# Kernel tuning notes

Hardware: AMD Instinct MI355X
Metric: run time of the kernel (lower is better)

Reference implementation:

```python
import jax, jax.numpy as jnp
import numpy as np

BN_EPS = 1e-5


def sparsemax(z):
    # z: [B, D]; sparse projection onto the simplex along last axis.
    D = z.shape[-1]
    z_sorted = jnp.flip(jnp.sort(z, axis=-1), axis=-1)          # descending
    cs = jnp.cumsum(z_sorted, axis=-1)                           # cumulative sums
    k = jnp.arange(1, D + 1, dtype=z.dtype)                      # 1..D
    support = (1.0 + k * z_sorted) > cs                          # support condition
    k_star = jnp.sum(support, axis=-1, keepdims=True)            # support size, int
    cs_k = jnp.take_along_axis(cs, k_star - 1, axis=-1)
    tau = (cs_k - 1.0) / k_star.astype(z.dtype)                  # threshold
    return jnp.maximum(z - tau, 0.0)


def setup_inputs() -> dict:
    key = jax.random.key(0)
    k1, k2, k3 = jax.random.split(key, 3)
    B, D = 32768, 1024
    a = jax.random.normal(k1, (B, D), dtype=jnp.float32)
    p = jax.random.uniform(k2, (B, D), dtype=jnp.float32)        # prior scales in (0,1)
    W = jax.random.normal(k3, (D, D), dtype=jnp.float32) * (1.0 / np.sqrt(D))
    b = jnp.zeros((D,), dtype=jnp.float32)
    gamma = jnp.ones((D,), dtype=jnp.float32)
    beta = jnp.zeros((D,), dtype=jnp.float32)
    return {"a": a, "p": p, "W": W, "b": b, "gamma": gamma, "beta": beta}


def reference(a, p, W, b, gamma, beta):
    # Linear: a @ W^T + b  (torch nn.Linear convention)
    h = jnp.einsum("bd,ed->be", a, W) + b
    # BatchNorm1d (training mode: batch stats, biased variance)
    mean = jnp.mean(h, axis=0)
    var = jnp.mean(jnp.square(h - mean), axis=0)
    h = (h - mean) * jax.lax.rsqrt(var + BN_EPS) * gamma + beta
    # Prior scaling, then sparsemax -> attention mask
    mask = sparsemax(p * h)
    return mask
```

## Files before the change

kernel.cpp:

```cpp
#include <hip/hip_runtime.h>
#include <hip/hip_fp16.h>
#include <stdint.h>

typedef _Float16 f16x8 __attribute__((ext_vector_type(8)));
typedef _Float16 f16x2 __attribute__((ext_vector_type(2)));
typedef float f32x4 __attribute__((ext_vector_type(4)));

#define BM 128
#define BN 128
#define BK 64

#define GBM 256
#define GBN 256
#define GBK 32

__device__ __forceinline__ void async_copy16(const void* g, void* l) {
  __builtin_amdgcn_global_load_lds(
      (__attribute__((address_space(1))) void*)(g),
      (__attribute__((address_space(3))) void*)(l),
      16, 0, 0);
}

__global__ __launch_bounds__(256) void cvt_f32_f16(const float* __restrict__ in,
                                                   _Float16* __restrict__ out,
                                                   size_t n8) {
  const size_t stride = (size_t)gridDim.x * 256;
  for (size_t i = (size_t)blockIdx.x * 256 + threadIdx.x; i < n8; i += stride) {
    const float4* s = (const float4*)in + i * 2;
    float4 u = s[0];
    float4 v = s[1];
    f16x8 h;
    h[0] = (_Float16)u.x; h[1] = (_Float16)u.y; h[2] = (_Float16)u.z; h[3] = (_Float16)u.w;
    h[4] = (_Float16)v.x; h[5] = (_Float16)v.y; h[6] = (_Float16)v.z; h[7] = (_Float16)v.w;
    ((f16x8*)out)[i] = h;
  }
}

__device__ __forceinline__ void stage32(const _Float16* __restrict__ src,
                                        _Float16* __restrict__ dst,
                                        int K, int wave, int lane) {
#pragma unroll
  for (int i = 0; i < 2; ++i) {
    const int basechunk = i * 512 + wave * 64;
    const int g   = basechunk + lane;
    const int row = g >> 2;
    const int sc  = (g & 3) ^ ((row >> 1) & 3);
    async_copy16(src + (size_t)row * K + sc * 8, dst + basechunk * 8);
  }
}

__global__ __launch_bounds__(512, 2) void gemm16(const _Float16* __restrict__ Ah,
                                                 const _Float16* __restrict__ Wh,
                                                 const float* __restrict__ bias,
                                                 _Float16* __restrict__ Hout,
                                                 float* __restrict__ psum,
                                                 float* __restrict__ psumsq,
                                                 int M, int N, int K) {
  __shared__ __attribute__((aligned(16))) _Float16 lsA[4][GBM * GBK];
  __shared__ __attribute__((aligned(16))) _Float16 lsB[4][GBN * GBK];

  const int tid  = threadIdx.x;
  const int wave = tid >> 6;
  const int lane = tid & 63;
  const int l16  = lane & 15;
  const int quad = lane >> 4;
  const int wr   = wave >> 2;
  const int wc   = wave & 3;

  const int li  = blockIdx.x;
  const int xcd = li & 7;
  const int jj  = li >> 3;
  const int bnT = jj & 3;
  const int bmT = xcd + (jj >> 2) * 8;
  const int bm  = bmT * GBM;
  const int bn  = bnT * GBN;

  const _Float16* Ag = Ah + (size_t)bm * K;
  const _Float16* Bg = Wh + (size_t)bn * K;

  f32x4 acc[8][4];
#pragma unroll
  for (int i = 0; i < 8; ++i)
#pragma unroll
    for (int j = 0; j < 4; ++j) acc[i][j] = (f32x4){0.f, 0.f, 0.f, 0.f};

  const int NT = K >> 5;

#pragma unroll
  for (int t = 0; t < 3; ++t) {
    stage32(Ag + t * GBK, lsA[t], K, wave, lane);
    stage32(Bg + t * GBK, lsB[t], K, wave, lane);
  }
  asm volatile("s_waitcnt vmcnt(8)" ::: "memory");
  __builtin_amdgcn_s_barrier();
  __builtin_amdgcn_sched_barrier(0);

  const int pos   = quad ^ ((l16 >> 1) & 3);
  const int abase = ((wr * 128 + l16) * 4 + pos) * 8;
  const int bbase = ((wc * 64 + l16) * 4 + pos) * 8;

#pragma unroll 1
  for (int t = 0; t < NT; ++t) {
    const _Float16* bufA = lsA[t & 3];
    const _Float16* bufB = lsB[t & 3];
    const int tp = t + 3;
    const bool st = tp < NT;

    if (st) stage32(Ag + (size_t)tp * GBK, lsA[tp & 3], K, wave, lane);
    f16x8 bf[4], af[4];
#pragma unroll
    for (int j = 0; j < 4; ++j) bf[j] = *(const f16x8*)&bufB[bbase + j * 512];
#pragma unroll
    for (int i = 0; i < 4; ++i) af[i] = *(const f16x8*)&bufA[abase + i * 512];
    __builtin_amdgcn_s_barrier();
    asm volatile("s_waitcnt lgkmcnt(0)" ::: "memory");
    __builtin_amdgcn_sched_barrier(0);
    __builtin_amdgcn_s_setprio(1);
#pragma unroll
    for (int i = 0; i < 4; ++i)
#pragma unroll
      for (int j = 0; j < 4; ++j)
        acc[i][j] = __builtin_amdgcn_mfma_f32_16x16x32_f16(af[i], bf[j], acc[i][j], 0, 0, 0);
    __builtin_amdgcn_s_setprio(0);
    __builtin_amdgcn_s_barrier();
    __builtin_amdgcn_sched_barrier(0);

    if (st) stage32(Bg + (size_t)tp * GBK, lsB[tp & 3], K, wave, lane);
    f16x8 af2[4];
#pragma unroll
    for (int i = 0; i < 4; ++i) af2[i] = *(const f16x8*)&bufA[abase + (i + 4) * 512];
    __builtin_amdgcn_s_barrier();
    asm volatile("s_waitcnt lgkmcnt(0)" ::: "memory");
    __builtin_amdgcn_sched_barrier(0);
    __builtin_amdgcn_s_setprio(1);
#pragma unroll
    for (int i = 0; i < 4; ++i)
#pragma unroll
      for (int j = 0; j < 4; ++j)
        acc[i + 4][j] = __builtin_amdgcn_mfma_f32_16x16x32_f16(af2[i], bf[j], acc[i + 4][j], 0, 0, 0);
    __builtin_amdgcn_s_setprio(0);

    if (t < NT - 3)       asm volatile("s_waitcnt vmcnt(8)" ::: "memory");
    else if (t == NT - 3) asm volatile("s_waitcnt vmcnt(4)" ::: "memory");
    else if (t == NT - 2) asm volatile("s_waitcnt vmcnt(0)" ::: "memory");
    __builtin_amdgcn_s_barrier();
    __builtin_amdgcn_sched_barrier(0);
  }

  f16x2* H2 = (f16x2*)Hout;
#pragma unroll
  for (int j = 0; j < 4; ++j) {
    const int c = bn + wc * 64 + j * 16 + l16;
    const float bv = bias[c];
    float s = 0.f, s2 = 0.f;
#pragma unroll
    for (int i = 0; i < 8; ++i) {
      const int r = bm + wr * 128 + i * 16 + quad * 4;
      f32x4 v = acc[i][j];
      const float v0 = v[0] + bv, v1 = v[1] + bv, v2 = v[2] + bv, v3 = v[3] + bv;
      s  += v0 + v1 + v2 + v3;
      s2 += v0 * v0 + v1 * v1 + v2 * v2 + v3 * v3;
      const size_t d0 = (size_t)(r >> 1) * N + c;
      H2[d0]     = (f16x2){(_Float16)v0, (_Float16)v1};
      H2[d0 + N] = (f16x2){(_Float16)v2, (_Float16)v3};
    }
    s  += __shfl_xor(s, 16, 64);  s  += __shfl_xor(s, 32, 64);
    s2 += __shfl_xor(s2, 16, 64); s2 += __shfl_xor(s2, 32, 64);
    if (quad == 0) {
      const size_t slot = (size_t)(bmT * 2 + wr) * N + c;
      psum[slot]   = s;
      psumsq[slot] = s2;
    }
  }
}

__global__ __launch_bounds__(256) void gemm_fallback(const float* __restrict__ Af,
                                                     const float* __restrict__ Wf,
                                                     const float* __restrict__ bias,
                                                     float* __restrict__ C,
                                                     float* __restrict__ sum,
                                                     float* __restrict__ sumsq,
                                                     int M, int N, int K) {
  __shared__ __attribute__((aligned(16))) _Float16 lsA[BM * BK];
  __shared__ __attribute__((aligned(16))) _Float16 lsB[BN * BK];
  const int tid  = threadIdx.x;
  const int wave = tid >> 6;
  const int lane = tid & 63;
  const int wrow = (wave >> 1) * 64;
  const int wcol = (wave & 1) * 64;
  const int l16  = lane & 15;
  const int quad = lane >> 4;
  const int bm = blockIdx.y * BM;
  const int bn = blockIdx.x * BN;

  f32x4 acc[4][4];
#pragma unroll
  for (int i = 0; i < 4; ++i)
#pragma unroll
    for (int j = 0; j < 4; ++j) acc[i][j] = (f32x4){0.f, 0.f, 0.f, 0.f};

  for (int k0 = 0; k0 < K; k0 += BK) {
#pragma unroll
    for (int i = 0; i < 4; ++i) {
      const int g   = i * 256 + tid;
      const int row = g >> 3;
      const int kc8 = g & 7;
      const int slot = row * 8 + (kc8 ^ (row & 7));
      {
        const float* src = Af + (size_t)(bm + row) * K + k0 + kc8 * 8;
        float4 u = *(const float4*)src;
        float4 v = *(const float4*)(src + 4);
        f16x8 h;
        h[0] = (_Float16)u.x; h[1] = (_Float16)u.y; h[2] = (_Float16)u.z; h[3] = (_Float16)u.w;
        h[4] = (_Float16)v.x; h[5] = (_Float16)v.y; h[6] = (_Float16)v.z; h[7] = (_Float16)v.w;
        *(f16x8*)&lsA[slot * 8] = h;
      }
      {
        const float* src = Wf + (size_t)(bn + row) * K + k0 + kc8 * 8;
        float4 u = *(const float4*)src;
        float4 v = *(const float4*)(src + 4);
        f16x8 h;
        h[0] = (_Float16)u.x; h[1] = (_Float16)u.y; h[2] = (_Float16)u.z; h[3] = (_Float16)u.w;
        h[4] = (_Float16)v.x; h[5] = (_Float16)v.y; h[6] = (_Float16)v.z; h[7] = (_Float16)v.w;
        *(f16x8*)&lsB[slot * 8] = h;
      }
    }
    __syncthreads();
#pragma unroll
    for (int kk = 0; kk < BK; kk += 32) {
      f16x8 af[4], bf[4];
#pragma unroll
      for (int i = 0; i < 4; ++i) {
        const int r = wrow + i * 16 + l16;
        const int col = ((kk >> 3) + quad) ^ (l16 & 7);
        af[i] = *(const f16x8*)&lsA[r * 64 + col * 8];
      }
#pragma unroll
      for (int j = 0; j < 4; ++j) {
        const int r = wcol + j * 16 + l16;
        const int col = ((kk >> 3) + quad) ^ (l16 & 7);
        bf[j] = *(const f16x8*)&lsB[r * 64 + col * 8];
      }
#pragma unroll
      for (int i = 0; i < 4; ++i)
#pragma unroll
        for (int j = 0; j < 4; ++j)
          acc[i][j] = __builtin_amdgcn_mfma_f32_16x16x32_f16(af[i], bf[j], acc[i][j], 0, 0, 0);
    }
    __syncthreads();
  }

#pragma unroll
  for (int j = 0; j < 4; ++j) {
    const int c = bn + wcol + j * 16 + l16;
    const float bv = bias[c];
    float s = 0.f, s2 = 0.f;
#pragma unroll
    for (int i = 0; i < 4; ++i) {
      const int r = bm + wrow + i * 16 + quad * 4;
      float* Cp = C + (size_t)r * N + c;
      f32x4 v = acc[i][j];
#pragma unroll
      for (int rr = 0; rr < 4; ++rr) {
        float val = v[rr] + bv;
        Cp[(size_t)rr * N] = val;
        s += val;
        s2 += val * val;
      }
    }
    s  += __shfl_xor(s, 16, 64);  s  += __shfl_xor(s, 32, 64);
    s2 += __shfl_xor(s2, 16, 64); s2 += __shfl_xor(s2, 32, 64);
    if (quad == 0) {
      atomicAdd(&sum[c], s);
      atomicAdd(&sumsq[c], s2);
    }
  }
}

__global__ __launch_bounds__(256) void bn_finalize_wave(const float* __restrict__ psum,
                                                        const float* __restrict__ psumsq,
                                                        const float* __restrict__ gamma,
                                                        const float* __restrict__ beta,
                                                        float* __restrict__ scale,
                                                        float* __restrict__ shift,
                                                        float invB, int S, int D) {
  const int wave = threadIdx.x >> 6;
  const int lane = threadIdx.x & 63;
  const int c = blockIdx.x * 4 + wave;
  float s = 0.f, q = 0.f;
  for (int u = lane; u < S; u += 64) {
    s += psum[(size_t)u * D + c];
    q += psumsq[(size_t)u * D + c];
  }
#pragma unroll
  for (int o = 32; o > 0; o >>= 1) {
    s += __shfl_xor(s, o, 64);
    q += __shfl_xor(q, o, 64);
  }
  if (lane == 0) {
    float mean = s * invB;
    float var  = q * invB - mean * mean;
    float rstd = rsqrtf(var + 1e-5f);
    float sc = rstd * gamma[c];
    scale[c] = sc;
    shift[c] = beta[c] - mean * sc;
  }
}

__global__ __launch_bounds__(256) void bn_finalize(const float* __restrict__ sum,
                                                   const float* __restrict__ sumsq,
                                                   const float* __restrict__ gamma,
                                                   const float* __restrict__ beta,
                                                   float* __restrict__ scale,
                                                   float* __restrict__ shift,
                                                   float invB) {
  const int c = blockIdx.x * 256 + threadIdx.x;
  float mean = sum[c] * invB;
  float var  = sumsq[c] * invB - mean * mean;
  float rstd = rsqrtf(var + 1e-5f);
  float sc = rstd * gamma[c];
  scale[c] = sc;
  shift[c] = beta[c] - mean * sc;
}

__global__ __launch_bounds__(256) void bn_sparsemax_h2(const _Float16* __restrict__ H2,
                                                       const float* __restrict__ P,
                                                       const float* __restrict__ scale,
                                                       const float* __restrict__ shift,
                                                       float* __restrict__ out, int D) {
  const int wave = threadIdx.x >> 6;
  const int lane = threadIdx.x & 63;
  const int row = blockIdx.x * 4 + wave;
  const int rp  = row >> 1;
  const int par = row & 1;

  const f16x8* Hc = (const f16x8*)(H2 + (size_t)rp * 2 * D);
  const f32x4* P4 = (const f32x4*)(P + (size_t)row * D);
  const f32x4* SC = (const f32x4*)scale;
  const f32x4* SH = (const f32x4*)shift;

  f32x4 z[4];
  float tot = 0.f;
#pragma unroll
  for (int j = 0; j < 4; ++j) {
    const int idx = j * 64 + lane;
    f16x8 h = Hc[idx];
    f32x4 hv = {(float)h[par], (float)h[2 + par], (float)h[4 + par], (float)h[6 + par]};
    f32x4 zz = P4[idx] * (hv * SC[idx] + SH[idx]);
    z[j] = zz;
    tot += zz[0] + zz[1] + zz[2] + zz[3];
  }
#pragma unroll
  for (int o = 32; o > 0; o >>= 1) tot += __shfl_xor(tot, o, 64);

  float tau = (tot - 1.0f) / (float)D;
  float kprev = -1.0f;
  for (int it = 0; it < 64; ++it) {
    float s = 0.f, kf = 0.f;
#pragma unroll
    for (int j = 0; j < 4; ++j)
#pragma unroll
      for (int c = 0; c < 4; ++c) {
        float zz = z[j][c];
        if (zz > tau) { s += zz; kf += 1.0f; }
      }
#pragma unroll
    for (int o = 32; o > 0; o >>= 1) {
      s  += __shfl_xor(s, o, 64);
      kf += __shfl_xor(kf, o, 64);
    }
    tau = (s - 1.0f) / kf;
    if (kf == kprev) break;
    kprev = kf;
  }

  f32x4* O4 = (f32x4*)(out + (size_t)row * D);
#pragma unroll
  for (int j = 0; j < 4; ++j) {
    const int idx = j * 64 + lane;
    f32x4 o;
#pragma unroll
    for (int c = 0; c < 4; ++c) o[c] = fmaxf(z[j][c] - tau, 0.f);
    O4[idx] = o;
  }
}

__global__ __launch_bounds__(256) void bn_sparsemax_f32(const float* __restrict__ H,
                                                        const float* __restrict__ P,
                                                        const float* __restrict__ scale,
                                                        const float* __restrict__ shift,
                                                        float* __restrict__ out, int D) {
  const int wave = threadIdx.x >> 6;
  const int lane = threadIdx.x & 63;
  const int row = blockIdx.x * 4 + wave;
  const size_t rowoff = (size_t)row * D;
  const f32x4* H4 = (const f32x4*)(H + rowoff);
  const f32x4* P4 = (const f32x4*)(P + rowoff);
  const f32x4* SC = (const f32x4*)scale;
  const f32x4* SH = (const f32x4*)shift;

  f32x4 z[4];
  float tot = 0.f;
#pragma unroll
  for (int j = 0; j < 4; ++j) {
    const int idx = j * 64 + lane;
    f32x4 zz = P4[idx] * (H4[idx] * SC[idx] + SH[idx]);
    z[j] = zz;
    tot += zz[0] + zz[1] + zz[2] + zz[3];
  }
#pragma unroll
  for (int o = 32; o > 0; o >>= 1) tot += __shfl_xor(tot, o, 64);

  float tau = (tot - 1.0f) / (float)D;
  float kprev = -1.0f;
  for (int it = 0; it < 64; ++it) {
    float s = 0.f, kf = 0.f;
#pragma unroll
    for (int j = 0; j < 4; ++j)
#pragma unroll
      for (int c = 0; c < 4; ++c) {
        float zz = z[j][c];
        if (zz > tau) { s += zz; kf += 1.0f; }
      }
#pragma unroll
    for (int o = 32; o > 0; o >>= 1) {
      s  += __shfl_xor(s, o, 64);
      kf += __shfl_xor(kf, o, 64);
    }
    tau = (s - 1.0f) / kf;
    if (kf == kprev) break;
    kprev = kf;
  }

  f32x4* O4 = (f32x4*)(out + rowoff);
#pragma unroll
  for (int j = 0; j < 4; ++j) {
    const int idx = j * 64 + lane;
    f32x4 o;
#pragma unroll
    for (int c = 0; c < 4; ++c) o[c] = fmaxf(z[j][c] - tau, 0.f);
    O4[idx] = o;
  }
}

extern "C" void kernel_launch(void* const* d_in, const int* in_sizes, int n_in,
                              void* d_out, int out_size, void* d_ws, size_t ws_size,
                              hipStream_t stream) {
  const float* a     = (const float*)d_in[0];
  const float* p     = (const float*)d_in[1];
  const float* W     = (const float*)d_in[2];
  const float* b     = (const float*)d_in[3];
  const float* gamma = (const float*)d_in[4];
  const float* beta  = (const float*)d_in[5];
  float* out = (float*)d_out;

  const int D = in_sizes[3];
  const int Brows = in_sizes[0] / D;
  const int K = D, N = D;
  const size_t na = (size_t)Brows * D;
  const size_t nw = (size_t)D * D;
  const int S = (Brows / GBM) * 2;

  const size_t statsB = (size_t)D * S * sizeof(float);
  float* psum   = (float*)d_ws;
  float* psumsq = (float*)((char*)d_ws + statsB);
  float* wscale = (float*)((char*)d_ws + 2 * statsB);
  float* wshift = wscale + D;
  const size_t off_Wh = 2 * statsB + 16384;
  _Float16* Wh = (_Float16*)((char*)d_ws + off_Wh);
  _Float16* H2 = Wh + nw;
  const size_t need = off_Wh + (nw + na) * sizeof(_Float16);
  _Float16* Ah = (_Float16*)d_out;

  const bool shape_ok = (Brows % GBM) == 0 && ((Brows / GBM) % 8) == 0 &&
                        (N / GBN) == 4 && (N % GBN) == 0 &&
                        (K % GBK) == 0 && (K / GBK) >= 4;

  if (ws_size >= need && shape_ok) {
    cvt_f32_f16<<<dim3(512), 256, 0, stream>>>(W, Wh, nw / 8);
    cvt_f32_f16<<<dim3(2048), 256, 0, stream>>>(a, Ah, na / 8);
    gemm16<<<dim3((Brows / GBM) * (N / GBN)), 512, 0, stream>>>(
        Ah, Wh, b, H2, psum, psumsq, Brows, N, K);
    bn_finalize_wave<<<dim3(D / 4), 256, 0, stream>>>(psum, psumsq, gamma, beta,
                                                      wscale, wshift,
                                                      1.0f / (float)Brows, S, D);
    bn_sparsemax_h2<<<dim3(Brows / 4), 256, 0, stream>>>(H2, p, wscale, wshift, out, D);
  } else {
    float* wsum   = (float*)d_ws;
    float* wsumsq = wsum + D;
    float* fscale = wsum + 2 * D;
    float* fshift = wsum + 3 * D;
    hipMemsetAsync(d_ws, 0, 2 * D * sizeof(float), stream);
    gemm_fallback<<<dim3(N / BN, Brows / BM), 256, 0, stream>>>(
        a, W, b, out, wsum, wsumsq, Brows, N, K);
    bn_finalize<<<dim3(D / 256), 256, 0, stream>>>(wsum, wsumsq, gamma, beta, fscale, fshift,
                                                   1.0f / (float)Brows);
    bn_sparsemax_f32<<<dim3(Brows / 4), 256, 0, stream>>>(out, p, fscale, fshift, out, D);
  }
}
```

Baseline: 428.0 us.

## Fuse A fp32-to-fp16 conversion into GEMM LDS staging, drop separate convert pass

The GEMM now streams the fp32 activation tiles straight into LDS and converts them to fp16 at fragment-load time, instead of running a separate conversion kernel over the whole activation matrix first. This removes a full read and write of the 32768x1024 activation in a separate launch. The A tile now takes twice the LDS, so the pipeline drops from four buffers to three with a prefetch distance of two, and there are extra LDS reads plus conversion ALU work inside the main loop. The wait counts are adjusted to match.

Result: no change. 433.5 us (+1.3%).

```diff
diff --git a/kernel.cpp b/kernel.cpp
--- a/kernel.cpp
+++ b/kernel.cpp
@@ -36,9 +36,9 @@
   }
 }
 
-__device__ __forceinline__ void stage32(const _Float16* __restrict__ src,
-                                        _Float16* __restrict__ dst,
-                                        int K, int wave, int lane) {
+__device__ __forceinline__ void stage_b16(const _Float16* __restrict__ src,
+                                          _Float16* __restrict__ dst,
+                                          int K, int wave, int lane) {
 #pragma unroll
   for (int i = 0; i < 2; ++i) {
     const int basechunk = i * 512 + wave * 64;
@@ -49,15 +49,28 @@
   }
 }
 
-__global__ __launch_bounds__(512, 2) void gemm16(const _Float16* __restrict__ Ah,
+__device__ __forceinline__ void stage_a32(const float* __restrict__ src,
+                                          float* __restrict__ dst,
+                                          int K, int wave, int lane) {
+#pragma unroll
+  for (int i = 0; i < 4; ++i) {
+    const int basechunk = i * 512 + wave * 64;
+    const int g   = basechunk + lane;
+    const int row = g >> 3;
+    const int sc  = (g & 7) ^ (row & 7);
+    async_copy16(src + (size_t)row * K + sc * 4, dst + basechunk * 4);
+  }
+}
+
+__global__ __launch_bounds__(512, 2) void gemm16(const float* __restrict__ Af,
                                                  const _Float16* __restrict__ Wh,
                                                  const float* __restrict__ bias,
                                                  _Float16* __restrict__ Hout,
                                                  float* __restrict__ psum,
                                                  float* __restrict__ psumsq,
                                                  int M, int N, int K) {
-  __shared__ __attribute__((aligned(16))) _Float16 lsA[4][GBM * GBK];
-  __shared__ __attribute__((aligned(16))) _Float16 lsB[4][GBN * GBK];
+  __shared__ __attribute__((aligned(16))) float    lsA[3][GBM * GBK];
+  __shared__ __attribute__((aligned(16))) _Float16 lsB[3][GBN * GBK];
 
   const int tid  = threadIdx.x;
   const int wave = tid >> 6;
@@ -75,7 +88,7 @@
   const int bm  = bmT * GBM;
   const int bn  = bnT * GBN;
 
-  const _Float16* Ag = Ah + (size_t)bm * K;
+  const float*    Ag = Af + (size_t)bm * K;
   const _Float16* Bg = Wh + (size_t)bn * K;
 
   f32x4 acc[8][4];
@@ -87,31 +100,42 @@
   const int NT = K >> 5;
 
 #pragma unroll
-  for (int t = 0; t < 3; ++t) {
-    stage32(Ag + t * GBK, lsA[t], K, wave, lane);
-    stage32(Bg + t * GBK, lsB[t], K, wave, lane);
-  }
-  asm volatile("s_waitcnt vmcnt(8)" ::: "memory");
+  for (int t = 0; t < 2; ++t) {
+    stage_a32(Ag + t * GBK, lsA[t], K, wave, lane);
+    stage_b16(Bg + t * GBK, lsB[t], K, wave, lane);
+  }
+  asm volatile("s_waitcnt vmcnt(6)" ::: "memory");
   __builtin_amdgcn_s_barrier();
   __builtin_amdgcn_sched_barrier(0);
 
-  const int pos   = quad ^ ((l16 >> 1) & 3);
-  const int abase = ((wr * 128 + l16) * 4 + pos) * 8;
-  const int bbase = ((wc * 64 + l16) * 4 + pos) * 8;
-
+  const int arow = wr * 128 + l16;
+  const int apos = (quad << 1) ^ (l16 & 7);
+  const int bbase = ((wc * 64 + l16) * 4 + (quad ^ ((l16 >> 1) & 3))) * 8;
+
+  int cur = 0;
 #pragma unroll 1
   for (int t = 0; t < NT; ++t) {
-    const _Float16* bufA = lsA[t & 3];
-    const _Float16* bufB = lsB[t & 3];
-    const int tp = t + 3;
-    const bool st = tp < NT;
-
-    if (st) stage32(Ag + (size_t)tp * GBK, lsA[tp & 3], K, wave, lane);
+    const float*    bufA = lsA[cur];
+    const _Float16* bufB = lsB[cur];
+    const int sb = (cur == 0) ? 2 : cur - 1;
+    const bool st = t + 2 < NT;
+
+    if (st) stage_a32(Ag + (size_t)(t + 2) * GBK, lsA[sb], K, wave, lane);
     f16x8 bf[4], af[4];
 #pragma unroll
     for (int j = 0; j < 4; ++j) bf[j] = *(const f16x8*)&bufB[bbase + j * 512];
 #pragma unroll
-    for (int i = 0; i < 4; ++i) af[i] = *(const f16x8*)&bufA[abase + i * 512];
+    for (int i = 0; i < 4; ++i) {
+      const int cbase = (arow + i * 16) * 8;
+      f32x4 a0 = *(const f32x4*)&bufA[(cbase + apos) * 4];
+      f32x4 a1 = *(const f32x4*)&bufA[(cbase + (apos ^ 1)) * 4];
+      f16x8 h;
+      h[0] = (_Float16)a0[0]; h[1] = (_Float16)a0[1];
+      h[2] = (_Float16)a0[2]; h[3] = (_Float16)a0[3];
+      h[4] = (_Float16)a1[0]; h[5] = (_Float16)a1[1];
+      h[6] = (_Float16)a1[2]; h[7] = (_Float16)a1[3];
+      af[i] = h;
+    }
     __builtin_amdgcn_s_barrier();
     asm volatile("s_waitcnt lgkmcnt(0)" ::: "memory");
     __builtin_amdgcn_sched_barrier(0);
@@ -125,10 +149,20 @@
     __builtin_amdgcn_s_barrier();
     __builtin_amdgcn_sched_barrier(0);
 
-    if (st) stage32(Bg + (size_t)tp * GBK, lsB[tp & 3], K, wave, lane);
+    if (st) stage_b16(Bg + (size_t)(t + 2) * GBK, lsB[sb], K, wave, lane);
     f16x8 af2[4];
 #pragma unroll
-    for (int i = 0; i < 4; ++i) af2[i] = *(const f16x8*)&bufA[abase + (i + 4) * 512];
+    for (int i = 0; i < 4; ++i) {
+      const int cbase = (arow + (i + 4) * 16) * 8;
+      f32x4 a0 = *(const f32x4*)&bufA[(cbase + apos) * 4];
+      f32x4 a1 = *(const f32x4*)&bufA[(cbase + (apos ^ 1)) * 4];
+      f16x8 h;
+      h[0] = (_Float16)a0[0]; h[1] = (_Float16)a0[1];
+      h[2] = (_Float16)a0[2]; h[3] = (_Float16)a0[3];
+      h[4] = (_Float16)a1[0]; h[5] = (_Float16)a1[1];
+      h[6] = (_Float16)a1[2]; h[7] = (_Float16)a1[3];
+      af2[i] = h;
+    }
     __builtin_amdgcn_s_barrier();
     asm volatile("s_waitcnt lgkmcnt(0)" ::: "memory");
     __builtin_amdgcn_sched_barrier(0);
@@ -140,11 +174,12 @@
         acc[i + 4][j] = __builtin_amdgcn_mfma_f32_16x16x32_f16(af2[i], bf[j], acc[i + 4][j], 0, 0, 0);
     __builtin_amdgcn_s_setprio(0);
 
-    if (t < NT - 3)       asm volatile("s_waitcnt vmcnt(8)" ::: "memory");
-    else if (t == NT - 3) asm volatile("s_waitcnt vmcnt(4)" ::: "memory");
+    if (t < NT - 2)       asm volatile("s_waitcnt vmcnt(6)" ::: "memory");
     else if (t == NT - 2) asm volatile("s_waitcnt vmcnt(0)" ::: "memory");
     __builtin_amdgcn_s_barrier();
     __builtin_amdgcn_sched_barrier(0);
+
+    cur = (cur == 2) ? 0 : cur + 1;
   }
 
   f16x2* H2 = (f16x2*)Hout;
@@ -470,7 +505,6 @@
   _Float16* Wh = (_Float16*)((char*)d_ws + off_Wh);
   _Float16* H2 = Wh + nw;
   const size_t need = off_Wh + (nw + na) * sizeof(_Float16);
-  _Float16* Ah = (_Float16*)d_out;
 
   const bool shape_ok = (Brows % GBM) == 0 && ((Brows / GBM) % 8) == 0 &&
                         (N / GBN) == 4 && (N % GBN) == 0 &&
@@ -478,9 +512,8 @@
 
   if (ws_size >= need && shape_ok) {
     cvt_f32_f16<<<dim3(512), 256, 0, stream>>>(W, Wh, nw / 8);
-    cvt_f32_f16<<<dim3(2048), 256, 0, stream>>>(a, Ah, na / 8);
     gemm16<<<dim3((Brows / GBM) * (N / GBN)), 512, 0, stream>>>(
-        Ah, Wh, b, H2, psum, psumsq, Brows, N, K);
+        a, Wh, b, H2, psum, psumsq, Brows, N, K);
     bn_finalize_wave<<<dim3(D / 4), 256, 0, stream>>>(psum, psumsq, gamma, beta,
                                                       wscale, wshift,
                                                       1.0f / (float)Brows, S, D);
```
